# Kernel tuning notes

Hardware: AMD Instinct MI355X
Metric: run time of the kernel (lower is better)

## Reference

```python
import jax, jax.numpy as jnp
import numpy as np

DIM = 1024
HID = 4096
NH = 16
HD = DIM // NH
B, S = 4, 2048
EPS = 1e-5
NEG = -1e9  # stand-in for -inf causal mask fill (numerically safe)


def layer_norm(x, g, b):
    mu = jnp.mean(x, axis=-1, keepdims=True)
    var = jnp.mean((x - mu) ** 2, axis=-1, keepdims=True)
    return (x - mu) * jax.lax.rsqrt(var + EPS) * g + b


def setup_inputs() -> dict:
    key = jax.random.key(0)
    ks = jax.random.split(key, 8)
    x = jax.random.normal(ks[0], (B, S, DIM), dtype=jnp.float32)
    # causal additive mask, broadcastable to [B, NH, S, S]
    causal = jnp.tril(jnp.ones((S, S), dtype=bool))
    mask = jnp.where(causal, 0.0, NEG).astype(jnp.float32)[None, None]
    sc = 1.0 / np.sqrt(DIM)
    wq = jax.random.normal(ks[1], (DIM, DIM), dtype=jnp.float32) * sc
    wk = jax.random.normal(ks[2], (DIM, DIM), dtype=jnp.float32) * sc
    wv = jax.random.normal(ks[3], (DIM, DIM), dtype=jnp.float32) * sc
    wo = jax.random.normal(ks[4], (DIM, DIM), dtype=jnp.float32) * sc
    w1 = jax.random.normal(ks[5], (DIM, HID), dtype=jnp.float32) * sc
    w2 = jax.random.normal(ks[6], (HID, DIM), dtype=jnp.float32) * (1.0 / np.sqrt(HID))
    ln1_w = jnp.ones((DIM,), jnp.float32); ln1_b = jnp.zeros((DIM,), jnp.float32)
    ln2_w = jnp.ones((DIM,), jnp.float32); ln2_b = jnp.zeros((DIM,), jnp.float32)
    return {"x": x, "mask": mask, "wq": wq, "wk": wk, "wv": wv, "wo": wo,
            "w1": w1, "w2": w2, "ln1_w": ln1_w, "ln1_b": ln1_b,
            "ln2_w": ln2_w, "ln2_b": ln2_b}


def reference(x, mask, wq, wk, wv, wo, w1, w2, ln1_w, ln1_b, ln2_w, ln2_b):
    b, s, _ = x.shape
    # pre-norm attention
    xn = layer_norm(x, ln1_w, ln1_b)
    q = (xn @ wq).reshape(b, s, NH, HD)
    k = (xn @ wk).reshape(b, s, NH, HD)
    v = (xn @ wv).reshape(b, s, NH, HD)
    scores = jnp.einsum('bqhd,bkhd->bhqk', q, k) / np.sqrt(HD) + mask
    probs = jax.nn.softmax(scores.astype(jnp.float32), axis=-1).astype(x.dtype)
    attn = jnp.einsum('bhqk,bkhd->bqhd', probs, v).reshape(b, s, NH * HD)
    h = x + attn @ wo
    # pre-norm ReLU FFN
    hn = layer_norm(h, ln2_w, ln2_b)
    ff = jax.nn.relu((hn @ w1).astype(jnp.float32)).astype(x.dtype) @ w2
    return h + ff
```

## Files before the change

kernel.cpp:

```cpp
#include <hip/hip_runtime.h>
#include <hip/hip_bf16.h>
#include <type_traits>

#define DIM 1024
#define HID 4096
#define NH 16
#define HD 64
#define BB 4
#define SS 2048
#define NROW (BB*SS)

typedef __attribute__((ext_vector_type(8))) short short8;
typedef __attribute__((ext_vector_type(4))) short short4v;
typedef __attribute__((ext_vector_type(4))) float f32x4;

__device__ __forceinline__ void gload16(const void* src, void* lds) {
  __builtin_amdgcn_global_load_lds(
      (const __attribute__((address_space(1))) unsigned int*)src,
      (__attribute__((address_space(3))) unsigned int*)lds, 16, 0, 0);
}
__device__ __forceinline__ short f2b(float f) {
  return __builtin_bit_cast(short, __float2bfloat16(f));
}
__device__ __forceinline__ float b2f(short s) {
  return __uint_as_float(((unsigned)(unsigned short)s) << 16);
}

__global__ __launch_bounds__(256) void ln_k(const float* __restrict__ x,
                                            const float* __restrict__ g,
                                            const float* __restrict__ bta,
                                            short* __restrict__ out) {
  int row = blockIdx.x;
  int t = threadIdx.x;
  int lane = t & 63, wid = t >> 6;
  float4 v = *(const float4*)(x + (size_t)row*DIM + t*4);
  float f[4] = {v.x, v.y, v.z, v.w};
  float s1 = 0.f, s2 = 0.f;
#pragma unroll
  for (int j = 0; j < 4; j++) { s1 += f[j]; s2 += f[j]*f[j]; }
#pragma unroll
  for (int off = 32; off > 0; off >>= 1) { s1 += __shfl_xor(s1, off); s2 += __shfl_xor(s2, off); }
  __shared__ float red[8];
  if (lane == 0) { red[wid] = s1; red[4+wid] = s2; }
  __syncthreads();
  s1 = red[0]+red[1]+red[2]+red[3];
  s2 = red[4]+red[5]+red[6]+red[7];
  float mu = s1 * (1.0f/DIM);
  float var = s2 * (1.0f/DIM) - mu*mu;
  float rs = rsqrtf(var + 1e-5f);
  float4 gv = *(const float4*)(g + t*4);
  float4 bv = *(const float4*)(bta + t*4);
  short4v o;
  o[0] = f2b((f[0]-mu)*rs*gv.x + bv.x);
  o[1] = f2b((f[1]-mu)*rs*gv.y + bv.y);
  o[2] = f2b((f[2]-mu)*rs*gv.z + bv.z);
  o[3] = f2b((f[3]-mu)*rs*gv.w + bv.w);
  *(short4v*)(out + (size_t)row*DIM + t*4) = o;
}

__global__ __launch_bounds__(256) void transp_f2b(const float* __restrict__ in, short* __restrict__ out,
                                                  int R, int C) {
  __shared__ __align__(16) short tile[64][72];
  int r0 = blockIdx.x*64, c0 = blockIdx.y*64;
  int t = threadIdx.x;
  int cr = t >> 4;
  int cc4 = (t & 15) * 4;
#pragma unroll
  for (int i = 0; i < 4; i++) {
    float4 v = *(const float4*)(in + (size_t)(r0 + cr + i*16)*C + c0 + cc4);
    tile[cr + i*16][cc4 + 0] = f2b(v.x);
    tile[cr + i*16][cc4 + 1] = f2b(v.y);
    tile[cr + i*16][cc4 + 2] = f2b(v.z);
    tile[cr + i*16][cc4 + 3] = f2b(v.w);
  }
  __syncthreads();
  int rr = t >> 3, cc = (t & 7) * 8;
#pragma unroll
  for (int i = 0; i < 2; i++) {
    int oc = rr + i*32;
    short8 v;
#pragma unroll
    for (int j = 0; j < 8; j++) v[j] = tile[cc + j][oc];
    *(short8*)(out + (size_t)(c0 + oc)*R + r0 + cc) = v;
  }
}

__global__ __launch_bounds__(256) void vtrans(const short* __restrict__ qkv, short* __restrict__ vt) {
  __shared__ __align__(16) short tile[64][72];
  int s0 = blockIdx.x*64;
  int z = blockIdx.y; int b = z >> 4, h = z & 15;
  int t = threadIdx.x;
  int rr = t >> 3, cc = (t & 7) * 8;
#pragma unroll
  for (int i = 0; i < 2; i++) {
    short8 v = *(const short8*)(qkv + (size_t)(b*SS + s0 + rr + i*32)*(3*DIM) + 2*DIM + h*HD + cc);
    *(short8*)&tile[rr + i*32][cc] = v;
  }
  __syncthreads();
#pragma unroll
  for (int i = 0; i < 2; i++) {
    int d = rr + i*32;
    short8 v;
#pragma unroll
    for (int j = 0; j < 8; j++) v[j] = tile[cc + j][d];
    *(short8*)(vt + ((size_t)z*HD + d)*SS + s0 + cc) = v;
  }
}

template<int EPI, typename CT>
__global__ __launch_bounds__(512) void gemm_bt(const short* __restrict__ A, int lda,
                                               const short* __restrict__ Bt, int ldb,
                                               CT* C, int ldc,
                                               const float* Res, int ldr,
                                               int K) {
  __shared__ __align__(16) short ldsA[128*64];
  __shared__ __align__(16) short ldsB[128*64];
  int t = threadIdx.x, lane = t & 63, wid = t >> 6;
  int bm = blockIdx.x*128, bn = blockIdx.y*128;
  int wr = wid >> 2, wc = wid & 3;
  f32x4 z4 = {0.f, 0.f, 0.f, 0.f};
  f32x4 acc[4][2];
#pragma unroll
  for (int m = 0; m < 4; m++)
#pragma unroll
    for (int n = 0; n < 2; n++) acc[m][n] = z4;
  const int srcCol = (((t & 7) ^ ((t >> 3) & 7)) * 8);
  const short* pa = A + (size_t)(bm + (t >> 3))*lda + srcCol;
  const short* pb = Bt + (size_t)(bn + (t >> 3))*ldb + srcCol;
  const int rowXor = (lane & 7) << 3;
  for (int k0 = 0; k0 < K; k0 += 64) {
    gload16(pa,                   &ldsA[wid*512]);
    gload16(pa + (size_t)64*lda,  &ldsA[4096 + wid*512]);
    gload16(pb,                   &ldsB[wid*512]);
    gload16(pb + (size_t)64*ldb,  &ldsB[4096 + wid*512]);
    pa += 64; pb += 64;
    __syncthreads();
    short8 af[4][2], bfr[2][2];
#pragma unroll
    for (int m = 0; m < 4; m++) {
      int row = wr*64 + m*16 + (lane & 15);
#pragma unroll
      for (int kk = 0; kk < 2; kk++)
        af[m][kk] = *(const short8*)&ldsA[row*64 + ((kk*32 + (lane >> 4)*8) ^ rowXor)];
    }
#pragma unroll
    for (int n = 0; n < 2; n++) {
      int row = wc*32 + n*16 + (lane & 15);
#pragma unroll
      for (int kk = 0; kk < 2; kk++)
        bfr[n][kk] = *(const short8*)&ldsB[row*64 + ((kk*32 + (lane >> 4)*8) ^ rowXor)];
    }
#pragma unroll
    for (int m = 0; m < 4; m++)
#pragma unroll
      for (int n = 0; n < 2; n++)
#pragma unroll
        for (int kk = 0; kk < 2; kk++)
          acc[m][n] = __builtin_amdgcn_mfma_f32_16x16x32_bf16(af[m][kk], bfr[n][kk], acc[m][n], 0, 0, 0);
    __syncthreads();
  }
#pragma unroll
  for (int m = 0; m < 4; m++) {
    int r0 = bm + wr*64 + m*16 + ((lane >> 4) << 2);
#pragma unroll
    for (int n = 0; n < 2; n++) {
      int c = bn + wc*32 + n*16 + (lane & 15);
#pragma unroll
      for (int r = 0; r < 4; r++) {
        float v = acc[m][n][r];
        if constexpr (EPI == 1) v = fmaxf(v, 0.0f);
        if constexpr (EPI == 3) v += Res[(size_t)(r0 + r)*ldr + c];
        if constexpr (std::is_same<CT, float>::value)
          C[(size_t)(r0 + r)*ldc + c] = v;
        else
          C[(size_t)(r0 + r)*ldc + c] = f2b(v);
      }
    }
  }
}

__global__ __launch_bounds__(512) void attn_k(short* qkv, const short* __restrict__ vt) {
  __shared__ __align__(16) short ldsK[2][64*64];
  __shared__ __align__(16) short ldsV[2][64*64];
  __shared__ __align__(16) short ldsP[8][16*64];
  int t = threadIdx.x, lane = t & 63, wid = t >> 6;
  int wgid = blockIdx.x;
  int xcd = wgid & 7, idx = wgid >> 3;
  int z  = xcd*8 + (idx & 7);
  int qi = 15 - (idx >> 3);
  int q0 = qi*128;
  int b = z >> 4, h = z & 15;
  const int ld = 3*DIM;
  const float SCALE2 = 0.125f * 1.44269504f;
  const float THR2   = 8.0f * 1.44269504f;
  const int half = wid >> 2;
  const int myq = q0 + wid*16;
  short8 qf[2];
  {
    const short* qp = qkv + (size_t)(b*SS + myq + (lane & 15))*ld + h*HD + (lane >> 4)*8;
    qf[0] = *(const short8*)qp;
    qf[1] = *(const short8*)(qp + 32);
  }
  f32x4 z4 = {0.f, 0.f, 0.f, 0.f};
  f32x4 accO[4];
#pragma unroll
  for (int n = 0; n < 4; n++) accO[n] = z4;
  float m_r[4], lp[4];
#pragma unroll
  for (int r = 0; r < 4; r++) { m_r[r] = -1e30f; lp[r] = 0.f; }
  const int srcCol = (((lane & 7) ^ ((lane >> 3) & 7)) * 8);
  const int rowXor = (lane & 7) << 3;
  int ntiles = 2*qi + 2;

  auto STAGE = [&](int it, int bsel) {
    int kv0 = it*64;
    const short* sk = qkv + (size_t)(b*SS + kv0 + (t >> 3))*ld + DIM + h*HD + srcCol;
    gload16(sk, &ldsK[bsel][wid*512]);
    const short* sv = vt + ((size_t)z*HD + (t >> 3))*SS + kv0 + srcCol;
    gload16(sv, &ldsV[bsel][wid*512]);
  };

  STAGE(0, 0);
  __syncthreads();
  for (int it = 0; it < ntiles; ++it) {
    int cur = it & 1;
    if (it + 1 < ntiles) STAGE(it + 1, cur ^ 1);
    int kv0 = it*64;
    if (it <= 2*qi + half) {
      f32x4 sacc[4];
#pragma unroll
      for (int n = 0; n < 4; n++) sacc[n] = z4;
      __builtin_amdgcn_s_setprio(1);
#pragma unroll
      for (int n = 0; n < 4; n++) {
#pragma unroll
        for (int kk = 0; kk < 2; kk++) {
          int colK = (kk*32 + (lane >> 4)*8) ^ rowXor;
          short8 kb = *(const short8*)&ldsK[cur][(n*16 + (lane & 15))*64 + colK];
          sacc[n] = __builtin_amdgcn_mfma_f32_16x16x32_bf16(qf[kk], kb, sacc[n], 0, 0, 0);
        }
      }
      __builtin_amdgcn_s_setprio(0);
      if (it == 2*qi + half) {
#pragma unroll
        for (int n = 0; n < 4; n++) {
          int kg = kv0 + n*16 + (lane & 15);
#pragma unroll
          for (int r = 0; r < 4; r++) {
            int qg = myq + ((lane >> 4) << 2) + r;
            sacc[n][r] = (kg <= qg) ? sacc[n][r] : -1e30f;
          }
        }
      }
      float mxs[4];
      float dmax = -1e30f;
#pragma unroll
      for (int r = 0; r < 4; r++) {
        float mx = fmaxf(fmaxf(sacc[0][r], sacc[1][r]), fmaxf(sacc[2][r], sacc[3][r]));
#pragma unroll
        for (int off = 1; off < 16; off <<= 1) mx = fmaxf(mx, __shfl_xor(mx, off));
        mxs[r] = mx * SCALE2;
        dmax = fmaxf(dmax, mxs[r] - m_r[r]);
      }
      if (__any(dmax > THR2)) {
#pragma unroll
        for (int r = 0; r < 4; r++) {
          float mn = fmaxf(m_r[r], mxs[r]);
          float al = exp2f(m_r[r] - mn);
          m_r[r] = mn;
          lp[r] *= al;
#pragma unroll
          for (int n = 0; n < 4; n++) accO[n][r] *= al;
        }
      }
#pragma unroll
      for (int r = 0; r < 4; r++) {
        float mn = m_r[r];
        float rs = 0.f;
#pragma unroll
        for (int n = 0; n < 4; n++) {
          float p = exp2f(fmaf(sacc[n][r], SCALE2, -mn));
          sacc[n][r] = p;
          rs += p;
        }
        lp[r] += rs;
      }
#pragma unroll
      for (int n = 0; n < 4; n++)
#pragma unroll
        for (int r = 0; r < 4; r++) {
          int prow = ((lane >> 4) << 2) + r;
          int pcol = (n*16 + (lane & 15)) ^ ((prow & 7) << 3);
          ldsP[wid][prow*64 + pcol] = f2b(sacc[n][r]);
        }
      __builtin_amdgcn_s_setprio(1);
#pragma unroll
      for (int nn = 0; nn < 4; nn++) {
#pragma unroll
        for (int kk = 0; kk < 2; kk++) {
          int colP = (kk*32 + (lane >> 4)*8) ^ rowXor;
          short8 vb  = *(const short8*)&ldsV[cur][(nn*16 + (lane & 15))*64 + colP];
          short8 pfr = *(const short8*)&ldsP[wid][(lane & 15)*64 + colP];
          accO[nn] = __builtin_amdgcn_mfma_f32_16x16x32_bf16(pfr, vb, accO[nn], 0, 0, 0);
        }
      }
      __builtin_amdgcn_s_setprio(0);
    }
    __syncthreads();
  }
  {
    float rl[4];
#pragma unroll
    for (int r = 0; r < 4; r++) {
      float l = lp[r];
#pragma unroll
      for (int off = 1; off < 16; off <<= 1) l += __shfl_xor(l, off);
      rl[r] = 1.0f / l;
    }
#pragma unroll
    for (int nn = 0; nn < 4; nn++) {
#pragma unroll
      for (int r = 0; r < 4; r++) {
        int qg = myq + ((lane >> 4) << 2) + r;
        float ov = accO[nn][r] * rl[r];
        qkv[(size_t)(b*SS + qg)*ld + 2*DIM + h*HD + nn*16 + (lane & 15)] = f2b(ov);
      }
    }
  }
}

extern "C" void kernel_launch(void* const* d_in, const int* in_sizes, int n_in,
                              void* d_out, int out_size, void* d_ws, size_t ws_size,
                              hipStream_t stream) {
  (void)in_sizes; (void)n_in; (void)out_size; (void)ws_size;
  const float* x    = (const float*)d_in[0];
  const float* wq   = (const float*)d_in[2];
  const float* wk   = (const float*)d_in[3];
  const float* wv   = (const float*)d_in[4];
  const float* wo   = (const float*)d_in[5];
  const float* w1   = (const float*)d_in[6];
  const float* w2   = (const float*)d_in[7];
  const float* ln1w = (const float*)d_in[8];
  const float* ln1b = (const float*)d_in[9];
  const float* ln2w = (const float*)d_in[10];
  const float* ln2b = (const float*)d_in[11];
  float* out = (float*)d_out;

  short* ws = (short*)d_ws;
  size_t o = 0;
  short* wqkvT = ws + o; o += (size_t)3*DIM*DIM;
  short* woT   = ws + o; o += (size_t)DIM*DIM;
  short* w1T   = ws + o; o += (size_t)HID*DIM;
  short* w2T   = ws + o; o += (size_t)DIM*HID;
  short* xn    = ws + o; o += (size_t)NROW*DIM;
  short* qkv   = ws + o; o += (size_t)NROW*3*DIM;
  short* ff1   = ws + o; o += (size_t)NROW*HID;
  short* vtb   = ff1;

  dim3 B256(256), B512(512);
  transp_f2b<<<dim3(16,16), B256, 0, stream>>>(wq, wqkvT,             DIM, DIM);
  transp_f2b<<<dim3(16,16), B256, 0, stream>>>(wk, wqkvT + DIM*DIM,   DIM, DIM);
  transp_f2b<<<dim3(16,16), B256, 0, stream>>>(wv, wqkvT + 2*DIM*DIM, DIM, DIM);
  transp_f2b<<<dim3(16,16), B256, 0, stream>>>(wo, woT, DIM, DIM);
  transp_f2b<<<dim3(16,64), B256, 0, stream>>>(w1, w1T, DIM, HID);
  transp_f2b<<<dim3(64,16), B256, 0, stream>>>(w2, w2T, HID, DIM);
  ln_k<<<NROW, B256, 0, stream>>>(x, ln1w, ln1b, xn);
  gemm_bt<0, short><<<dim3(NROW/128, 3*DIM/128), B512, 0, stream>>>(xn, DIM, wqkvT, DIM, qkv, 3*DIM, nullptr, 0, DIM);
  vtrans<<<dim3(SS/64, BB*NH), B256, 0, stream>>>(qkv, vtb);
  attn_k<<<dim3(1024), B512, 0, stream>>>(qkv, vtb);
  gemm_bt<3, float><<<dim3(NROW/128, DIM/128), B512, 0, stream>>>(qkv + 2*DIM, 3*DIM, woT, DIM, out, DIM, x, DIM, DIM);
  ln_k<<<NROW, B256, 0, stream>>>(out, ln2w, ln2b, xn);
  gemm_bt<1, short><<<dim3(NROW/128, HID/128), B512, 0, stream>>>(xn, DIM, w1T, DIM, ff1, HID, nullptr, 0, DIM);
  gemm_bt<3, float><<<dim3(NROW/128, DIM/128), B512, 0, stream>>>(ff1, HID, w2T, HID, out, DIM, out, DIM, HID);
}
```

Baseline: 408.6 us.

## Warp-specialize GEMM with producer waves feeding double-buffered LDS tiles

Each GEMM block gains two extra waves: one streams A tiles and one streams B tiles into double-buffered LDS through global_load_lds, prefetching the next K-tile while the eight compute waves run MFMAs on the current one. The compute waves no longer issue global loads, and they raise their scheduling priority around the MFMA section. The aim is to hide global-load latency that the old single-buffered loop exposed at every barrier. In exchange, LDS per block doubles, blocks grow to 640 threads, and only two waves issue all the loads, which may limit occupancy and load throughput.

```diff
diff --git a/kernel.cpp b/kernel.cpp
--- a/kernel.cpp
+++ b/kernel.cpp
@@ -108,15 +108,39 @@
 }
 
 template<int EPI, typename CT>
-__global__ __launch_bounds__(512) void gemm_bt(const short* __restrict__ A, int lda,
+__global__ __launch_bounds__(640) void gemm_bt(const short* __restrict__ A, int lda,
                                                const short* __restrict__ Bt, int ldb,
                                                CT* C, int ldc,
                                                const float* Res, int ldr,
                                                int K) {
-  __shared__ __align__(16) short ldsA[128*64];
-  __shared__ __align__(16) short ldsB[128*64];
+  __shared__ __align__(16) short ldsA[2][128*64];
+  __shared__ __align__(16) short ldsB[2][128*64];
   int t = threadIdx.x, lane = t & 63, wid = t >> 6;
   int bm = blockIdx.x*128, bn = blockIdx.y*128;
+  const int nt = K >> 6;
+
+  if (wid >= 8) {
+    const short* base = (wid == 8) ? (A + (size_t)bm*lda) : (Bt + (size_t)bn*ldb);
+    const int ldx = (wid == 8) ? lda : ldb;
+    short* d0 = (wid == 8) ? ldsA[0] : ldsB[0];
+    short* d1 = (wid == 8) ? ldsA[1] : ldsB[1];
+    const int srcCol = (((lane & 7) ^ (lane >> 3)) * 8);
+    const short* p = base + (size_t)(lane >> 3)*ldx + srcCol;
+#pragma unroll
+    for (int j = 0; j < 16; j++) gload16(p + (size_t)(j*8)*ldx, d0 + j*512);
+    __syncthreads();
+    for (int tt = 0; tt < nt; tt++) {
+      if (tt + 1 < nt) {
+        const short* pn = p + (size_t)(tt + 1)*64;
+        short* d = ((tt + 1) & 1) ? d1 : d0;
+#pragma unroll
+        for (int j = 0; j < 16; j++) gload16(pn + (size_t)(j*8)*ldx, d + j*512);
+      }
+      __syncthreads();
+    }
+    return;
+  }
+
   int wr = wid >> 2, wc = wid & 3;
   f32x4 z4 = {0.f, 0.f, 0.f, 0.f};
   f32x4 acc[4][2];
@@ -124,32 +148,27 @@
   for (int m = 0; m < 4; m++)
 #pragma unroll
     for (int n = 0; n < 2; n++) acc[m][n] = z4;
-  const int srcCol = (((t & 7) ^ ((t >> 3) & 7)) * 8);
-  const short* pa = A + (size_t)(bm + (t >> 3))*lda + srcCol;
-  const short* pb = Bt + (size_t)(bn + (t >> 3))*ldb + srcCol;
   const int rowXor = (lane & 7) << 3;
-  for (int k0 = 0; k0 < K; k0 += 64) {
-    gload16(pa,                   &ldsA[wid*512]);
-    gload16(pa + (size_t)64*lda,  &ldsA[4096 + wid*512]);
-    gload16(pb,                   &ldsB[wid*512]);
-    gload16(pb + (size_t)64*ldb,  &ldsB[4096 + wid*512]);
-    pa += 64; pb += 64;
-    __syncthreads();
+  __syncthreads();
+  for (int tt = 0; tt < nt; tt++) {
+    const short* bA = ldsA[tt & 1];
+    const short* bB = ldsB[tt & 1];
     short8 af[4][2], bfr[2][2];
 #pragma unroll
     for (int m = 0; m < 4; m++) {
       int row = wr*64 + m*16 + (lane & 15);
 #pragma unroll
       for (int kk = 0; kk < 2; kk++)
-        af[m][kk] = *(const short8*)&ldsA[row*64 + ((kk*32 + (lane >> 4)*8) ^ rowXor)];
+        af[m][kk] = *(const short8*)&bA[row*64 + ((kk*32 + (lane >> 4)*8) ^ rowXor)];
     }
 #pragma unroll
     for (int n = 0; n < 2; n++) {
       int row = wc*32 + n*16 + (lane & 15);
 #pragma unroll
       for (int kk = 0; kk < 2; kk++)
-        bfr[n][kk] = *(const short8*)&ldsB[row*64 + ((kk*32 + (lane >> 4)*8) ^ rowXor)];
-    }
+        bfr[n][kk] = *(const short8*)&bB[row*64 + ((kk*32 + (lane >> 4)*8) ^ rowXor)];
+    }
+    __builtin_amdgcn_s_setprio(1);
 #pragma unroll
     for (int m = 0; m < 4; m++)
 #pragma unroll
@@ -157,6 +176,7 @@
 #pragma unroll
         for (int kk = 0; kk < 2; kk++)
           acc[m][n] = __builtin_amdgcn_mfma_f32_16x16x32_bf16(af[m][kk], bfr[n][kk], acc[m][n], 0, 0, 0);
+    __builtin_amdgcn_s_setprio(0);
     __syncthreads();
   }
 #pragma unroll
@@ -357,7 +377,7 @@
   short* ff1   = ws + o; o += (size_t)NROW*HID;
   short* vtb   = ff1;
 
-  dim3 B256(256), B512(512);
+  dim3 B256(256), B512(512), B640(640);
   transp_f2b<<<dim3(16,16), B256, 0, stream>>>(wq, wqkvT,             DIM, DIM);
   transp_f2b<<<dim3(16,16), B256, 0, stream>>>(wk, wqkvT + DIM*DIM,   DIM, DIM);
   transp_f2b<<<dim3(16,16), B256, 0, stream>>>(wv, wqkvT + 2*DIM*DIM, DIM, DIM);
@@ -365,11 +385,11 @@
   transp_f2b<<<dim3(16,64), B256, 0, stream>>>(w1, w1T, DIM, HID);
   transp_f2b<<<dim3(64,16), B256, 0, stream>>>(w2, w2T, HID, DIM);
   ln_k<<<NROW, B256, 0, stream>>>(x, ln1w, ln1b, xn);
-  gemm_bt<0, short><<<dim3(NROW/128, 3*DIM/128), B512, 0, stream>>>(xn, DIM, wqkvT, DIM, qkv, 3*DIM, nullptr, 0, DIM);
+  gemm_bt<0, short><<<dim3(NROW/128, 3*DIM/128), B640, 0, stream>>>(xn, DIM, wqkvT, DIM, qkv, 3*DIM, nullptr, 0, DIM);
   vtrans<<<dim3(SS/64, BB*NH), B256, 0, stream>>>(qkv, vtb);
   attn_k<<<dim3(1024), B512, 0, stream>>>(qkv, vtb);
-  gemm_bt<3, float><<<dim3(NROW/128, DIM/128), B512, 0, stream>>>(qkv + 2*DIM, 3*DIM, woT, DIM, out, DIM, x, DIM, DIM);
+  gemm_bt<3, float><<<dim3(NROW/128, DIM/128), B640, 0, stream>>>(qkv + 2*DIM, 3*DIM, woT, DIM, out, DIM, x, DIM, DIM);
   ln_k<<<NROW, B256, 0, stream>>>(out, ln2w, ln2b, xn);
-  gemm_bt<1, short><<<dim3(NROW/128, HID/128), B512, 0, stream>>>(xn, DIM, w1T, DIM, ff1, HID, nullptr, 0, DIM);
-  gemm_bt<3, float><<<dim3(NROW/128, DIM/128), B512, 0, stream>>>(ff1, HID, w2T, HID, out, DIM, out, DIM, HID);
-}
+  gemm_bt<1, short><<<dim3(NROW/128, HID/128), B640, 0, stream>>>(xn, DIM, w1T, DIM, ff1, HID, nullptr, 0, DIM);
+  gemm_bt<3, float><<<dim3(NROW/128, DIM/128), B640, 0, stream>>>(ff1, HID, w2T, HID, out, DIM, out, DIM, HID);
+}
```

New measurement: 452.9 us. +10.9%, slower.
